# Optimization experiments

Measured on AMD Instinct MI355X. Metric: run time of the kernel, lower is better.

The kernel has to match this reference:

```python
import jax, jax.numpy as jnp
import numpy as np

N = 50000
IN_C, HID_C, OUT_C = 128, 256, 128
E = 800000


def sage_conv(x, edge_index, W_l, b_l, W_r, num_nodes):
    # PyG SAGEConv (aggr='mean'): out = lin_l(mean_{j in N(i)} x_j) + lin_r(x_i)
    src, dst = edge_index[0], edge_index[1]
    msgs = x[src]  # [E, C] gather of source features
    agg = jax.ops.segment_sum(msgs, dst, num_segments=num_nodes)  # [N, C]
    deg = jax.ops.segment_sum(jnp.ones((edge_index.shape[1],), x.dtype), dst,
                              num_segments=num_nodes)
    mean = agg / jnp.maximum(deg, 1.0)[:, None]
    return mean @ W_l.T + b_l + x @ W_r.T


def setup_inputs() -> dict:
    key = jax.random.key(0)
    ks = jax.random.split(key, 8)
    x = jax.random.normal(ks[0], (N, IN_C), dtype=jnp.float32)
    edge_index = jax.random.randint(ks[1], (2, E), 0, N, dtype=jnp.int64)
    s1 = 1.0 / np.sqrt(IN_C)
    s2 = 1.0 / np.sqrt(HID_C)
    W1_l = jax.random.uniform(ks[2], (HID_C, IN_C), jnp.float32, -s1, s1)
    W1_r = jax.random.uniform(ks[3], (HID_C, IN_C), jnp.float32, -s1, s1)
    b1 = jnp.zeros((HID_C,), jnp.float32)
    W2_l = jax.random.uniform(ks[4], (OUT_C, HID_C), jnp.float32, -s2, s2)
    W2_r = jax.random.uniform(ks[5], (OUT_C, HID_C), jnp.float32, -s2, s2)
    b2 = jnp.zeros((OUT_C,), jnp.float32)
    return {"x": x, "edge_index": edge_index,
            "W1_l": W1_l, "b1": b1, "W1_r": W1_r,
            "W2_l": W2_l, "b2": b2, "W2_r": W2_r}


def reference(x, edge_index, W1_l, b1, W1_r, W2_l, b2, W2_r):
    h = sage_conv(x, edge_index, W1_l, b1, W1_r, N)
    h = jax.nn.relu(h)
    # dropout p=0.5 is identity in eval mode (inference reference)
    out = sage_conv(h, edge_index, W2_l, b2, W2_r, N)
    return out
```

## Files before the change

### kernel.cpp

```cpp
#include <hip/hip_runtime.h>

#define NN   50000
#define INC  128
#define HIDC 256
#define OUTC 128
#define NE   800000
#define MP   50048
#define CAP  64

#define EPB 4096
#define NCH ((NE + EPB - 1) / EPB)
#define RSZ 6250

typedef short bfrag __attribute__((ext_vector_type(8)));
typedef float f32x4 __attribute__((ext_vector_type(4)));
typedef unsigned short us8 __attribute__((ext_vector_type(8)));

__device__ inline unsigned short f2b(float f) {
    union { float f; unsigned u; } v; v.f = f;
    unsigned u = v.u;
    return (unsigned short)((u + 0x7fffu + ((u >> 16) & 1u)) >> 16);
}
__device__ inline float b2f(unsigned short s) {
    union { unsigned u; float f; } v; v.u = ((unsigned)s) << 16;
    return v.f;
}

__global__ __launch_bounds__(256) void k_prep(
    const float* __restrict__ x, const float* __restrict__ W1l,
    const float* __restrict__ W1r, const float* __restrict__ W2l,
    const float* __restrict__ W2r, unsigned short* __restrict__ xb16,
    unsigned short* __restrict__ A1f, unsigned short* __restrict__ B1f,
    unsigned short* __restrict__ B2f, int* __restrict__ cnt) {
    const int b = blockIdx.x;
    if (b < 3125) {
        int t = b * 256 + threadIdx.x;
        int i = t >> 4;
        int c8 = t & 15;
        const float* src = x + (size_t)i * INC + c8 * 8;
        float4 v0 = *(const float4*)src;
        float4 v1 = *(const float4*)(src + 4);
        us8 o = { f2b(v0.x), f2b(v0.y), f2b(v0.z), f2b(v0.w),
                  f2b(v1.x), f2b(v1.y), f2b(v1.z), f2b(v1.w) };
        *(us8*)(xb16 + (size_t)i * INC + c8 * 8) = o;
        size_t off = (size_t)(i >> 4) * 4096 + (size_t)(4 + (c8 >> 2)) * 512
                   + (size_t)(c8 & 3) * 128 + (size_t)(i & 15) * 8;
        *(us8*)(A1f + off) = o;
    } else if (b < 3157) {
        int t = (b - 3125) * 256 + threadIdx.x;
        int n = t >> 5;
        int k8 = t & 31;
        int k = k8 * 8;
        const float* src = (k < 128) ? (W1l + (size_t)n * INC + k)
                                     : (W1r + (size_t)n * INC + (k - 128));
        float4 v0 = *(const float4*)src;
        float4 v1 = *(const float4*)(src + 4);
        us8 o = { f2b(v0.x), f2b(v0.y), f2b(v0.z), f2b(v0.w),
                  f2b(v1.x), f2b(v1.y), f2b(v1.z), f2b(v1.w) };
        size_t off = (size_t)(n >> 4) * 4096 + (size_t)(k8 >> 2) * 512
                   + (size_t)(k8 & 3) * 128 + (size_t)(n & 15) * 8;
        *(us8*)(B1f + off) = o;
    } else if (b < 3189) {
        int t = (b - 3157) * 256 + threadIdx.x;
        int n = t >> 5;
        int k8 = t & 31;
        const float* src = (n < 128) ? (W2l + (size_t)n * HIDC + k8 * 8)
                                     : (W2r + (size_t)(n - 128) * HIDC + k8 * 8);
        float4 v0 = *(const float4*)src;
        float4 v1 = *(const float4*)(src + 4);
        us8 o = { f2b(v0.x), f2b(v0.y), f2b(v0.z), f2b(v0.w),
                  f2b(v1.x), f2b(v1.y), f2b(v1.z), f2b(v1.w) };
        size_t off = (size_t)(n >> 4) * 4096 + (size_t)(k8 >> 2) * 512
                   + (size_t)(k8 & 3) * 128 + (size_t)(n & 15) * 8;
        *(us8*)(B2f + off) = o;
    } else {
        int t = (b - 3189) * 256 + threadIdx.x;
        if (t < (NN + 3) / 4) *(int4*)(cnt + t * 4) = make_int4(0, 0, 0, 0);
    }
}

__global__ __launch_bounds__(256) void k_fill(const int* __restrict__ ei,
                                              int* __restrict__ cnt,
                                              unsigned short* __restrict__ csr) {
    const int r = blockIdx.x & 7;
    const int c = blockIdx.x >> 3;
    const int lo = r * RSZ, hi = lo + RSZ;
    const int base = c * EPB + threadIdx.x;
#pragma unroll
    for (int i = 0; i < EPB / 256; ++i) {
        int e = base + i * 256;
        if (e < NE) {
            int dst = __builtin_nontemporal_load(ei + NE + e);
            if (dst >= lo && dst < hi) {
                int srcv = __builtin_nontemporal_load(ei + e);
                int old = atomicAdd(&cnt[dst], 1);
                if (old < CAP) csr[dst * CAP + old] = (unsigned short)srcv;
            }
        }
    }
}

__global__ __launch_bounds__(256) void k_gather_mean(
    const int* __restrict__ cnt, const unsigned short* __restrict__ csr,
    const unsigned short* __restrict__ xb16, unsigned short* __restrict__ A1f) {
    const int node = blockIdx.x * 4 + (threadIdx.x >> 6);
    const int lane = threadIdx.x & 63;
    const int sub = lane >> 4;
    const int cl = lane & 15;
    const int cn = cnt[node];
    const int m = (cn < CAP) ? cn : CAP;
    const unsigned short* cb = csr + node * CAP;
    float acc[8] = {};
    const unsigned short* xb = xb16 + cl * 8;
    int i = sub;
    for (; i + 4 < m; i += 8) {
        int s0 = cb[i], s1 = cb[i + 4];
        us8 v0 = *(const us8*)(xb + (size_t)s0 * INC);
        us8 v1 = *(const us8*)(xb + (size_t)s1 * INC);
#pragma unroll
        for (int j = 0; j < 8; ++j) acc[j] += b2f(v0[j]) + b2f(v1[j]);
    }
    if (i < m) {
        int s0 = cb[i];
        us8 v0 = *(const us8*)(xb + (size_t)s0 * INC);
#pragma unroll
        for (int j = 0; j < 8; ++j) acc[j] += b2f(v0[j]);
    }
#pragma unroll
    for (int j = 0; j < 8; ++j) {
        acc[j] += __shfl_xor(acc[j], 16, 64);
        acc[j] += __shfl_xor(acc[j], 32, 64);
    }
    if (sub == 0) {
        float inv = 1.0f / fmaxf((float)cn, 1.0f);
        us8 o;
#pragma unroll
        for (int j = 0; j < 8; ++j) o[j] = f2b(acc[j] * inv);
        size_t off = (size_t)(node >> 4) * 4096 + (size_t)(cl >> 2) * 512
                   + (size_t)(cl & 3) * 128 + (size_t)(node & 15) * 8;
        *(us8*)(A1f + off) = o;
    }
}

__global__ __launch_bounds__(256) void k_mgemm_fused(
    const unsigned short* __restrict__ A, const unsigned short* __restrict__ B1,
    const float* __restrict__ b1, const unsigned short* __restrict__ B2,
    const float* __restrict__ b2, unsigned short* __restrict__ HP,
    float* __restrict__ OUT) {
    __shared__ unsigned short Hsl[16384];
    const int tid = threadIdx.x;
    const int lane = tid & 63;
    const int w = tid >> 6;
    const int col = lane & 15, quad = lane >> 4;
    const int m0 = blockIdx.x * 64;

    {
        const us8* src = (const us8*)(A + (size_t)(m0 >> 4) * 4096);
        us8* dst = (us8*)Hsl;
#pragma unroll
        for (int i = 0; i < 8; ++i) dst[tid + i * 256] = src[tid + i * 256];
    }
    __syncthreads();

    f32x4 acc[4][4];
#pragma unroll
    for (int i = 0; i < 4; ++i)
#pragma unroll
        for (int j = 0; j < 4; ++j) acc[i][j] = (f32x4){0.f, 0.f, 0.f, 0.f};
#pragma unroll
    for (int kc = 0; kc < 8; ++kc) {
        bfrag a[4], b[4];
#pragma unroll
        for (int mt = 0; mt < 4; ++mt)
            a[mt] = *(const bfrag*)(Hsl + mt * 4096 + kc * 512 + quad * 128 + col * 8);
#pragma unroll
        for (int nt = 0; nt < 4; ++nt)
            b[nt] = *(const bfrag*)(B1 + (size_t)(w * 4 + nt) * 4096 + kc * 512 + quad * 128 + col * 8);
#pragma unroll
        for (int mt = 0; mt < 4; ++mt)
#pragma unroll
            for (int nt = 0; nt < 4; ++nt)
                acc[mt][nt] = __builtin_amdgcn_mfma_f32_16x16x32_bf16(a[mt], b[nt], acc[mt][nt], 0, 0, 0);
    }
    __syncthreads();

#pragma unroll
    for (int nt = 0; nt < 4; ++nt) {
        int n = w * 64 + nt * 16 + col;
        float bb = b1[n];
        int noff = (n >> 5) * 512 + ((n >> 3) & 3) * 128 + (n & 7);
#pragma unroll
        for (int mt = 0; mt < 4; ++mt) {
#pragma unroll
            for (int r = 0; r < 4; ++r) {
                int ml = quad * 4 + r;
                Hsl[mt * 4096 + noff + ml * 8] = f2b(fmaxf(acc[mt][nt][r] + bb, 0.f));
            }
        }
    }
    __syncthreads();

#pragma unroll
    for (int i = 0; i < 4; ++i)
#pragma unroll
        for (int j = 0; j < 4; ++j) acc[i][j] = (f32x4){0.f, 0.f, 0.f, 0.f};
#pragma unroll
    for (int kc = 0; kc < 8; ++kc) {
        bfrag a[4], b[4];
#pragma unroll
        for (int mt = 0; mt < 4; ++mt)
            a[mt] = *(const bfrag*)(Hsl + mt * 4096 + kc * 512 + quad * 128 + col * 8);
#pragma unroll
        for (int nt = 0; nt < 4; ++nt)
            b[nt] = *(const bfrag*)(B2 + (size_t)(w * 4 + nt) * 4096 + kc * 512 + quad * 128 + col * 8);
#pragma unroll
        for (int mt = 0; mt < 4; ++mt)
#pragma unroll
            for (int nt = 0; nt < 4; ++nt)
                acc[mt][nt] = __builtin_amdgcn_mfma_f32_16x16x32_bf16(a[mt], b[nt], acc[mt][nt], 0, 0, 0);
    }

    if (w < 2) {
#pragma unroll
        for (int mt = 0; mt < 4; ++mt)
#pragma unroll
            for (int nt = 0; nt < 4; ++nt) {
                int n = w * 64 + nt * 16 + col;
#pragma unroll
                for (int r = 0; r < 4; ++r) {
                    int m = m0 + mt * 16 + quad * 4 + r;
                    if (m < NN) HP[(size_t)m * OUTC + n] = f2b(acc[mt][nt][r]);
                }
            }
    } else {
#pragma unroll
        for (int mt = 0; mt < 4; ++mt)
#pragma unroll
            for (int nt = 0; nt < 4; ++nt) {
                int n = (w - 2) * 64 + nt * 16 + col;
                float bb = b2[n];
#pragma unroll
                for (int r = 0; r < 4; ++r) {
                    int m = m0 + mt * 16 + quad * 4 + r;
                    if (m < NN) OUT[(size_t)m * OUTC + n] = acc[mt][nt][r] + bb;
                }
            }
    }
}

__global__ __launch_bounds__(256) void k_gather_add(
    const int* __restrict__ cnt, const unsigned short* __restrict__ csr,
    const unsigned short* __restrict__ hp, float* __restrict__ out) {
    const int node = blockIdx.x * 4 + (threadIdx.x >> 6);
    const int lane = threadIdx.x & 63;
    const int sub = lane >> 4;
    const int cl = lane & 15;
    const int cn = cnt[node];
    const int m = (cn < CAP) ? cn : CAP;
    const unsigned short* cb = csr + node * CAP;
    float acc[8] = {};
    const unsigned short* hb = hp + cl * 8;
    int i = sub;
    for (; i + 4 < m; i += 8) {
        int s0 = cb[i], s1 = cb[i + 4];
        us8 v0 = *(const us8*)(hb + (size_t)s0 * OUTC);
        us8 v1 = *(const us8*)(hb + (size_t)s1 * OUTC);
#pragma unroll
        for (int j = 0; j < 8; ++j) acc[j] += b2f(v0[j]) + b2f(v1[j]);
    }
    if (i < m) {
        int s0 = cb[i];
        us8 v0 = *(const us8*)(hb + (size_t)s0 * OUTC);
#pragma unroll
        for (int j = 0; j < 8; ++j) acc[j] += b2f(v0[j]);
    }
#pragma unroll
    for (int j = 0; j < 8; ++j) {
        acc[j] += __shfl_xor(acc[j], 16, 64);
        acc[j] += __shfl_xor(acc[j], 32, 64);
    }
    if (sub == 0) {
        float inv = 1.0f / fmaxf((float)cn, 1.0f);
        float* p = out + (size_t)node * OUTC + cl * 8;
        float4 c0v = *(float4*)p;
        float4 c1v = *(float4*)(p + 4);
        c0v.x += acc[0] * inv; c0v.y += acc[1] * inv;
        c0v.z += acc[2] * inv; c0v.w += acc[3] * inv;
        c1v.x += acc[4] * inv; c1v.y += acc[5] * inv;
        c1v.z += acc[6] * inv; c1v.w += acc[7] * inv;
        *(float4*)p = c0v;
        *(float4*)(p + 4) = c1v;
    }
}

extern "C" void kernel_launch(void* const* d_in, const int* in_sizes, int n_in,
                              void* d_out, int out_size, void* d_ws, size_t ws_size,
                              hipStream_t stream) {
    const float* x   = (const float*)d_in[0];
    const int*   ei  = (const int*)d_in[1];
    const float* W1l = (const float*)d_in[2];
    const float* b1  = (const float*)d_in[3];
    const float* W1r = (const float*)d_in[4];
    const float* W2l = (const float*)d_in[5];
    const float* b2  = (const float*)d_in[6];
    const float* W2r = (const float*)d_in[7];
    float* out = (float*)d_out;

    int* cnt = (int*)d_ws;
    unsigned short* csr = (unsigned short*)(cnt + ((NN + 63) & ~63));
    unsigned short* A1f  = csr + (size_t)NN * CAP;
    unsigned short* xb16 = A1f + (size_t)MP * 256;
    unsigned short* hp   = xb16 + (size_t)NN * 128;
    unsigned short* B1f  = hp + (size_t)NN * 128;
    unsigned short* B2f  = B1f + 256 * 256;

    k_prep<<<3238, 256, 0, stream>>>(x, W1l, W1r, W2l, W2r, xb16, A1f, B1f, B2f, cnt);
    k_fill<<<NCH * 8, 256, 0, stream>>>(ei, cnt, csr);
    k_gather_mean<<<NN / 4, 256, 0, stream>>>(cnt, csr, xb16, A1f);

    k_mgemm_fused<<<MP / 64, 256, 0, stream>>>(A1f, B1f, b1, B2f, b2, hp, out);

    k_gather_add<<<NN / 4, 256, 0, stream>>>(cnt, csr, hp, out);
}
```

Baseline: 229.2 us.

## Fuse CSR fill into prep kernel, unroll gathers, use nontemporal prep traffic

Merges the edge-bucketing fill kernel and the bf16 conversion/prep kernel into one launch, so the fill blocks run concurrently with the conversion blocks. The count zeroing moves to a hipMemsetAsync beforehand. Prep loads and stores become nontemporal. Both gather kernels are unrolled to issue four independent row loads per iteration for more memory-level parallelism. The extra memset launch adds some overhead, and the nontemporal stores could evict data that the gather kernel re-reads soon after (xb16).

```diff
diff --git a/kernel.cpp b/kernel.cpp
--- a/kernel.cpp
+++ b/kernel.cpp
@@ -11,9 +11,11 @@
 #define EPB 4096
 #define NCH ((NE + EPB - 1) / EPB)
 #define RSZ 6250
+#define FILLB (NCH * 8)
 
 typedef short bfrag __attribute__((ext_vector_type(8)));
 typedef float f32x4 __attribute__((ext_vector_type(4)));
+typedef float f4 __attribute__((ext_vector_type(4)));
 typedef unsigned short us8 __attribute__((ext_vector_type(8)));
 
 __device__ inline unsigned short f2b(float f) {
@@ -26,77 +28,74 @@
     return v.f;
 }
 
-__global__ __launch_bounds__(256) void k_prep(
-    const float* __restrict__ x, const float* __restrict__ W1l,
-    const float* __restrict__ W1r, const float* __restrict__ W2l,
-    const float* __restrict__ W2r, unsigned short* __restrict__ xb16,
-    unsigned short* __restrict__ A1f, unsigned short* __restrict__ B1f,
-    unsigned short* __restrict__ B2f, int* __restrict__ cnt) {
+__global__ __launch_bounds__(256) void k_prefill(
+    const float* __restrict__ x, const int* __restrict__ ei,
+    const float* __restrict__ W1l, const float* __restrict__ W1r,
+    const float* __restrict__ W2l, const float* __restrict__ W2r,
+    unsigned short* __restrict__ xb16, unsigned short* __restrict__ A1f,
+    unsigned short* __restrict__ B1f, unsigned short* __restrict__ B2f,
+    int* __restrict__ cnt, unsigned short* __restrict__ csr) {
     const int b = blockIdx.x;
-    if (b < 3125) {
-        int t = b * 256 + threadIdx.x;
+    if (b < FILLB) {
+        const int r = b & 7;
+        const int c = b >> 3;
+        const int lo = r * RSZ, hi = lo + RSZ;
+        const int base = c * EPB + threadIdx.x;
+#pragma unroll
+        for (int i = 0; i < EPB / 256; ++i) {
+            int e = base + i * 256;
+            if (e < NE) {
+                int dst = __builtin_nontemporal_load(ei + NE + e);
+                if (dst >= lo && dst < hi) {
+                    int srcv = __builtin_nontemporal_load(ei + e);
+                    int old = atomicAdd(&cnt[dst], 1);
+                    if (old < CAP) csr[dst * CAP + old] = (unsigned short)srcv;
+                }
+            }
+        }
+        return;
+    }
+    const int pb = b - FILLB;
+    if (pb < 3125) {
+        int t = pb * 256 + threadIdx.x;
         int i = t >> 4;
         int c8 = t & 15;
         const float* src = x + (size_t)i * INC + c8 * 8;
-        float4 v0 = *(const float4*)src;
-        float4 v1 = *(const float4*)(src + 4);
+        f4 v0 = __builtin_nontemporal_load((const f4*)src);
+        f4 v1 = __builtin_nontemporal_load((const f4*)(src + 4));
         us8 o = { f2b(v0.x), f2b(v0.y), f2b(v0.z), f2b(v0.w),
                   f2b(v1.x), f2b(v1.y), f2b(v1.z), f2b(v1.w) };
-        *(us8*)(xb16 + (size_t)i * INC + c8 * 8) = o;
+        __builtin_nontemporal_store(o, (us8*)(xb16 + (size_t)i * INC + c8 * 8));
         size_t off = (size_t)(i >> 4) * 4096 + (size_t)(4 + (c8 >> 2)) * 512
                    + (size_t)(c8 & 3) * 128 + (size_t)(i & 15) * 8;
-        *(us8*)(A1f + off) = o;
-    } else if (b < 3157) {
-        int t = (b - 3125) * 256 + threadIdx.x;
+        __builtin_nontemporal_store(o, (us8*)(A1f + off));
+    } else if (pb < 3157) {
+        int t = (pb - 3125) * 256 + threadIdx.x;
         int n = t >> 5;
         int k8 = t & 31;
         int k = k8 * 8;
         const float* src = (k < 128) ? (W1l + (size_t)n * INC + k)
                                      : (W1r + (size_t)n * INC + (k - 128));
-        float4 v0 = *(const float4*)src;
-        float4 v1 = *(const float4*)(src + 4);
+        f4 v0 = __builtin_nontemporal_load((const f4*)src);
+        f4 v1 = __builtin_nontemporal_load((const f4*)(src + 4));
         us8 o = { f2b(v0.x), f2b(v0.y), f2b(v0.z), f2b(v0.w),
                   f2b(v1.x), f2b(v1.y), f2b(v1.z), f2b(v1.w) };
         size_t off = (size_t)(n >> 4) * 4096 + (size_t)(k8 >> 2) * 512
                    + (size_t)(k8 & 3) * 128 + (size_t)(n & 15) * 8;
-        *(us8*)(B1f + off) = o;
-    } else if (b < 3189) {
-        int t = (b - 3157) * 256 + threadIdx.x;
+        __builtin_nontemporal_store(o, (us8*)(B1f + off));
+    } else {
+        int t = (pb - 3157) * 256 + threadIdx.x;
         int n = t >> 5;
         int k8 = t & 31;
         const float* src = (n < 128) ? (W2l + (size_t)n * HIDC + k8 * 8)
                                      : (W2r + (size_t)(n - 128) * HIDC + k8 * 8);
-        float4 v0 = *(const float4*)src;
-        float4 v1 = *(const float4*)(src + 4);
+        f4 v0 = __builtin_nontemporal_load((const f4*)src);
+        f4 v1 = __builtin_nontemporal_load((const f4*)(src + 4));
         us8 o = { f2b(v0.x), f2b(v0.y), f2b(v0.z), f2b(v0.w),
                   f2b(v1.x), f2b(v1.y), f2b(v1.z), f2b(v1.w) };
         size_t off = (size_t)(n >> 4) * 4096 + (size_t)(k8 >> 2) * 512
                    + (size_t)(k8 & 3) * 128 + (size_t)(n & 15) * 8;
-        *(us8*)(B2f + off) = o;
-    } else {
-        int t = (b - 3189) * 256 + threadIdx.x;
-        if (t < (NN + 3) / 4) *(int4*)(cnt + t * 4) = make_int4(0, 0, 0, 0);
-    }
-}
-
-__global__ __launch_bounds__(256) void k_fill(const int* __restrict__ ei,
-                                              int* __restrict__ cnt,
-                                              unsigned short* __restrict__ csr) {
-    const int r = blockIdx.x & 7;
-    const int c = blockIdx.x >> 3;
-    const int lo = r * RSZ, hi = lo + RSZ;
-    const int base = c * EPB + threadIdx.x;
-#pragma unroll
-    for (int i = 0; i < EPB / 256; ++i) {
-        int e = base + i * 256;
-        if (e < NE) {
-            int dst = __builtin_nontemporal_load(ei + NE + e);
-            if (dst >= lo && dst < hi) {
-                int srcv = __builtin_nontemporal_load(ei + e);
-                int old = atomicAdd(&cnt[dst], 1);
-                if (old < CAP) csr[dst * CAP + old] = (unsigned short)srcv;
-            }
-        }
+        __builtin_nontemporal_store(o, (us8*)(B2f + off));
     }
 }
 
@@ -113,12 +112,23 @@
     float acc[8] = {};
     const unsigned short* xb = xb16 + cl * 8;
     int i = sub;
-    for (; i + 4 < m; i += 8) {
+    for (; i + 12 < m; i += 16) {
+        int s0 = cb[i], s1 = cb[i + 4], s2 = cb[i + 8], s3 = cb[i + 12];
+        us8 v0 = *(const us8*)(xb + (size_t)s0 * INC);
+        us8 v1 = *(const us8*)(xb + (size_t)s1 * INC);
+        us8 v2 = *(const us8*)(xb + (size_t)s2 * INC);
+        us8 v3 = *(const us8*)(xb + (size_t)s3 * INC);
+#pragma unroll
+        for (int j = 0; j < 8; ++j)
+            acc[j] += (b2f(v0[j]) + b2f(v1[j])) + (b2f(v2[j]) + b2f(v3[j]));
+    }
+    if (i + 4 < m) {
         int s0 = cb[i], s1 = cb[i + 4];
         us8 v0 = *(const us8*)(xb + (size_t)s0 * INC);
         us8 v1 = *(const us8*)(xb + (size_t)s1 * INC);
 #pragma unroll
         for (int j = 0; j < 8; ++j) acc[j] += b2f(v0[j]) + b2f(v1[j]);
+        i += 8;
     }
     if (i < m) {
         int s0 = cb[i];
@@ -261,12 +271,23 @@
     float acc[8] = {};
     const unsigned short* hb = hp + cl * 8;
     int i = sub;
-    for (; i + 4 < m; i += 8) {
+    for (; i + 12 < m; i += 16) {
+        int s0 = cb[i], s1 = cb[i + 4], s2 = cb[i + 8], s3 = cb[i + 12];
+        us8 v0 = *(const us8*)(hb + (size_t)s0 * OUTC);
+        us8 v1 = *(const us8*)(hb + (size_t)s1 * OUTC);
+        us8 v2 = *(const us8*)(hb + (size_t)s2 * OUTC);
+        us8 v3 = *(const us8*)(hb + (size_t)s3 * OUTC);
+#pragma unroll
+        for (int j = 0; j < 8; ++j)
+            acc[j] += (b2f(v0[j]) + b2f(v1[j])) + (b2f(v2[j]) + b2f(v3[j]));
+    }
+    if (i + 4 < m) {
         int s0 = cb[i], s1 = cb[i + 4];
         us8 v0 = *(const us8*)(hb + (size_t)s0 * OUTC);
         us8 v1 = *(const us8*)(hb + (size_t)s1 * OUTC);
 #pragma unroll
         for (int j = 0; j < 8; ++j) acc[j] += b2f(v0[j]) + b2f(v1[j]);
+        i += 8;
     }
     if (i < m) {
         int s0 = cb[i];
@@ -314,8 +335,10 @@
     unsigned short* B1f  = hp + (size_t)NN * 128;
     unsigned short* B2f  = B1f + 256 * 256;
 
-    k_prep<<<3238, 256, 0, stream>>>(x, W1l, W1r, W2l, W2r, xb16, A1f, B1f, B2f, cnt);
-    k_fill<<<NCH * 8, 256, 0, stream>>>(ei, cnt, csr);
+    (void)hipMemsetAsync(cnt, 0, (size_t)NN * sizeof(int), stream);
+
+    k_prefill<<<FILLB + 3189, 256, 0, stream>>>(x, ei, W1l, W1r, W2l, W2r,
+                                                xb16, A1f, B1f, B2f, cnt, csr);
     k_gather_mean<<<NN / 4, 256, 0, stream>>>(cnt, csr, xb16, A1f);
 
     k_mgemm_fused<<<MP / 64, 256, 0, stream>>>(A1f, B1f, b1, B2f, b2, hp, out);
```

New measurement: 230.1 us. Within noise of the previous version (+0.4%).
